# Kernel optimization log

Hardware: AMD Instinct MI355X
Metric: run time of the kernel (lower is better)

The kernel has to match this reference:

```python
import jax, jax.numpy as jnp
import numpy as np

LAMBDA_BOX = 5.0
LAMBDA_CLS = 1.0
NUM_CLASSES = 80


def setup_inputs() -> dict:
    key = jax.random.key(0)
    k1, k2, k3, k4, k5, k6 = jax.random.split(key, 6)
    B, P, T = 16, 16384, 64
    C = 5 + NUM_CLASSES
    raw = jax.random.normal(k1, (B, P, C), dtype=jnp.float32)
    # overwrite first 4 channels with valid xyxy boxes so IoU is meaningful
    p_xy = jax.random.uniform(k2, (B, P, 2), dtype=jnp.float32) * 448.0
    p_wh = jax.random.uniform(k3, (B, P, 2), dtype=jnp.float32) * 64.0 + 4.0
    raw = raw.at[..., :4].set(jnp.concatenate([p_xy, p_xy + p_wh], axis=-1))
    t_xy = jax.random.uniform(k4, (B, T, 2), dtype=jnp.float32) * 448.0
    t_wh = jax.random.uniform(k5, (B, T, 2), dtype=jnp.float32) * 64.0 + 4.0
    t_cls = jax.random.randint(k6, (B, T), 0, NUM_CLASSES).astype(jnp.float32)
    targets = jnp.concatenate([t_xy, t_xy + t_wh, t_cls[..., None]], axis=-1)
    return {"raw_preds": raw, "targets": targets, "epoch": 5}


def _iou_matrix(pb, tb):
    # pb: [B,P,4], tb: [B,T,4] -> IoU [B,P,T] (xyxy boxes)
    x1 = jnp.maximum(pb[:, :, None, 0], tb[:, None, :, 0])
    y1 = jnp.maximum(pb[:, :, None, 1], tb[:, None, :, 1])
    x2 = jnp.minimum(pb[:, :, None, 2], tb[:, None, :, 2])
    y2 = jnp.minimum(pb[:, :, None, 3], tb[:, None, :, 3])
    w = x2 - x1
    h = y2 - y1
    inter = w * h
    valid = (w > 0) & (h > 0)
    area_p = (pb[:, :, 2] - pb[:, :, 0]) * (pb[:, :, 3] - pb[:, :, 1])
    area_t = (tb[:, :, 2] - tb[:, :, 0]) * (tb[:, :, 3] - tb[:, :, 1])
    union = area_p[:, :, None] + area_t[:, None, :] - inter
    iou = jnp.where(valid & (union > 0), inter / jnp.where(union > 0, union, 1.0), 0.0)
    return iou


def _smooth_l1_sum(x, t):
    d = jnp.abs(x - t)
    return jnp.sum(jnp.where(d < 1.0, 0.5 * d * d, d - 0.5), axis=(-2, -1))


def _bce_logits_sum(x, t):
    # sum over last axis of BCEWithLogits
    return jnp.sum(jnp.logaddexp(0.0, x) - x * t, axis=-1)


def reference(raw_preds, targets, epoch):
    B, P, _ = raw_preds.shape
    T = targets.shape[1]
    # IoU is computed from detached numpy boxes in the original -> stop_gradient
    pb = jax.lax.stop_gradient(raw_preds[..., :4])
    tb = targets[..., :4]
    iou = _iou_matrix(pb, tb)                      # [B,P,T]
    # warmup branch (epoch < warmup_epochs): best pred per target
    matched_pred = jnp.argmax(iou, axis=1)         # [B,T]
    pred_pos_boxes = jnp.take_along_axis(raw_preds[..., :4], matched_pred[..., None], axis=1)  # [B,T,4]
    box_loss = _smooth_l1_sum(pred_pos_boxes, tb)  # [B]
    pred_pos_cls = jnp.take_along_axis(raw_preds[..., 5:], matched_pred[..., None], axis=1)    # [B,T,C]
    tcls = targets[..., 4].astype(jnp.int32)       # [B,T]
    logp = jax.nn.log_softmax(pred_pos_cls, axis=-1)
    cls_loss = -jnp.sum(jnp.take_along_axis(logp, tcls[..., None], axis=-1), axis=(-2, -1))    # [B]
    conf_target = jax.vmap(lambda idx: jnp.zeros((P,), jnp.float32).at[idx].set(1.0))(matched_pred)  # [B,P]
    conf_loss = _bce_logits_sum(raw_preds[..., 4], conf_target)  # [B]
    per_sample = LAMBDA_BOX * box_loss + LAMBDA_CLS * cls_loss + conf_loss
    return jnp.sum(per_sample) / B
```

## Files before the change

kernel.cpp:

```cpp
#include <hip/hip_runtime.h>
#include <math.h>

#define BB 16
#define PP 16384
#define TT 64
#define CC 85
#define WPW 64
#define PRED_PER_BLK 256
#define NSLOT 64

typedef float float4u __attribute__((ext_vector_type(4), aligned(4)));


__global__ __launch_bounds__(256) void pass1_kernel(const float* __restrict__ raw,
                                                    const float* __restrict__ tgt,
                                                    float2* __restrict__ cand,
                                                    float* __restrict__ conf_part) {
#pragma clang fp contract(off)
    int b     = blockIdx.x >> 6;
    int chunk = blockIdx.x & 63;
    int wave  = threadIdx.x >> 6;
    int lane  = threadIdx.x & 63;
    int p0    = chunk * PRED_PER_BLK + wave * WPW;

    __shared__ float4 sbox[4][WPW];
    __shared__ float  sarea[4][WPW];
    __shared__ float  sval[4][WPW];
    __shared__ int    sidx[4][WPW];
    __shared__ float  sconf[4];

    {
        const float* pr = raw + ((size_t)b * PP + p0 + lane) * CC;
        float4u bx = *(const float4u*)pr;
        float c = pr[4];
        sbox[wave][lane]  = make_float4(bx.x, bx.y, bx.z, bx.w);
        sarea[wave][lane] = (bx.z - bx.x) * (bx.w - bx.y);
        float ca = fmaxf(c, 0.0f) + log1pf(expf(-fabsf(c)));
        for (int m = 32; m > 0; m >>= 1) ca += __shfl_xor(ca, m);
        if (lane == 0) sconf[wave] = ca;
    }

    const float* trow = tgt + (size_t)(b * TT + lane) * 5;
    float tx1 = trow[0], ty1 = trow[1], tx2 = trow[2], ty2 = trow[3];
    float area_t = (tx2 - tx1) * (ty2 - ty1);

    float best = -1.0f;
    int bidx = 0;
#pragma unroll 4
    for (int j = 0; j < WPW; ++j) {
        float4 pb = sbox[wave][j];
        float ap  = sarea[wave][j];
        float x1 = fmaxf(pb.x, tx1), y1 = fmaxf(pb.y, ty1);
        float x2 = fminf(pb.z, tx2), y2 = fminf(pb.w, ty2);
        float w = x2 - x1, h = y2 - y1;
        float inter = w * h;
        bool valid = (w > 0.0f) && (h > 0.0f);
        float uni = (ap + area_t) - inter;
        float iou = (valid && (uni > 0.0f)) ? (inter / uni) : 0.0f;
        if (iou > best) { best = iou; bidx = p0 + j; }
    }
    sval[wave][lane] = best;
    sidx[wave][lane] = bidx;
    __syncthreads();

    if (threadIdx.x == 0)
        conf_part[blockIdx.x] = (sconf[0] + sconf[1]) + (sconf[2] + sconf[3]);

    if (wave == 0) {
        float v = sval[0][lane];
        int   i = sidx[0][lane];
        for (int w2 = 1; w2 < 4; ++w2) {
            float v2 = sval[w2][lane];
            int   i2 = sidx[w2][lane];
            if (v2 > v || (v2 == v && i2 < i)) { v = v2; i = i2; }
        }
        cand[(size_t)(b * TT + lane) * NSLOT + chunk] = make_float2(v, __int_as_float(i));
    }
}

__global__ __launch_bounds__(64) void pass2_kernel(const float* __restrict__ raw,
                                                   const float* __restrict__ tgt,
                                                   const float2* __restrict__ cand,
                                                   float* __restrict__ loss_bt,
                                                   int* __restrict__ matched) {
#pragma clang fp contract(off)
    int bt = blockIdx.x;
    int b = bt >> 6;
    int lane = threadIdx.x;

    float2 c2 = cand[(size_t)bt * NSLOT + lane];
    float v = c2.x;
    int idx = __float_as_int(c2.y);
    for (int m = 1; m < 64; m <<= 1) {
        float ov = __shfl_xor(v, m);
        int   oi = __shfl_xor(idx, m);
        if (ov > v || (ov == v && oi < idx)) { v = ov; idx = oi; }
    }
    const float* prow = raw + ((size_t)b * PP + idx) * CC;
    float l0 = prow[5 + lane];
    float l1 = (lane < 16) ? prow[69 + lane] : -INFINITY;
    float mx = fmaxf(l0, l1);
    for (int m = 1; m < 64; m <<= 1) mx = fmaxf(mx, __shfl_xor(mx, m));
    float e = expf(l0 - mx) + ((lane < 16) ? expf(l1 - mx) : 0.0f);
    for (int m = 1; m < 64; m <<= 1) e += __shfl_xor(e, m);

    if (lane == 0) {
        const float* trow = tgt + (size_t)bt * 5;
        int tcls = (int)trow[4];
        float cls = (mx + logf(e)) - prow[5 + tcls];
        float s = 0.0f;
        for (int k = 0; k < 4; ++k) {
            float d = fabsf(prow[k] - trow[k]);
            s += (d < 1.0f) ? 0.5f * d * d : (d - 0.5f);
        }
        loss_bt[bt] = 5.0f * s + cls;
        matched[bt] = idx;
    }
}

__global__ __launch_bounds__(256) void pass3_kernel(const float* __restrict__ raw,
                                                    const float* __restrict__ conf_part,
                                                    const float* __restrict__ loss_bt,
                                                    const int* __restrict__ matched,
                                                    float* __restrict__ out) {
    __shared__ int sm[BB * TT];
    __shared__ float red[256];
    int tid = threadIdx.x;
    for (int i = tid; i < BB * TT; i += 256) sm[i] = matched[i];
    __syncthreads();

    float acc = 0.0f;
    for (int i = tid; i < BB * TT; i += 256) {
        int m = sm[i];
        bool first = true;
        for (int t2 = i & ~63; t2 < i; ++t2)
            if (sm[t2] == m) { first = false; break; }
        int b = i >> 6;
        float sub = first ? raw[((size_t)b * PP + m) * CC + 4] : 0.0f;
        acc += loss_bt[i] - sub;
    }
    for (int i = tid; i < 1024; i += 256) acc += conf_part[i];

    red[tid] = acc;
    __syncthreads();
    for (int s = 128; s > 0; s >>= 1) {
        if (tid < s) red[tid] += red[tid + s];
        __syncthreads();
    }
    if (tid == 0) out[0] = red[0] / (float)BB;
}

extern "C" void kernel_launch(void* const* d_in, const int* in_sizes, int n_in,
                              void* d_out, int out_size, void* d_ws, size_t ws_size,
                              hipStream_t stream) {
    const float* raw = (const float*)d_in[0];
    const float* tgt = (const float*)d_in[1];
    float* out = (float*)d_out;
    float* wsf = (float*)d_ws;

    float2* cand    = (float2*)wsf;
    float*  conf_p  = wsf + 131072;
    float*  loss_bt = wsf + 132096;
    int*    match   = (int*)(wsf + 133120);

    pass1_kernel<<<BB * 64, 256, 0, stream>>>(raw, tgt, cand, conf_p);
    pass2_kernel<<<BB * TT, 64, 0, stream>>>(raw, tgt, cand, loss_bt, match);
    pass3_kernel<<<1, 256, 0, stream>>>(raw, conf_p, loss_bt, match, out);
}
```

Before: 53.25 us.

## Fuse pass2 and pass3 into single-block tail kernel and double pass1 chunk size

Pass1 now handles 512 predictions per block, halving the block count and the number of candidate slots per target. It also stores candidates chunk-major so reads are coalesced. The former per-target pass2 and final reduction pass3 are merged into one 1024-thread kernel. In that kernel each thread reduces its target's candidates, computes the log-softmax and box loss with vectorized loads, handles the duplicate-match correction, and reduces everything. This removes a kernel launch and the intermediate workspace round trip. The cost is that all tail work runs on one block, with 80-wide per-thread loops and uncoalesced gathers.

```diff
diff --git a/kernel.cpp b/kernel.cpp
--- a/kernel.cpp
+++ b/kernel.cpp
@@ -5,9 +5,9 @@
 #define PP 16384
 #define TT 64
 #define CC 85
-#define WPW 64
-#define PRED_PER_BLK 256
-#define NSLOT 64
+#define PRED_PER_BLK 512
+#define CHUNKS (PP / PRED_PER_BLK)
+#define NBLK1 (BB * CHUNKS)
 
 typedef float float4u __attribute__((ext_vector_type(4), aligned(4)));
 
@@ -17,28 +17,32 @@
                                                     float2* __restrict__ cand,
                                                     float* __restrict__ conf_part) {
 #pragma clang fp contract(off)
-    int b     = blockIdx.x >> 6;
-    int chunk = blockIdx.x & 63;
-    int wave  = threadIdx.x >> 6;
-    int lane  = threadIdx.x & 63;
-    int p0    = chunk * PRED_PER_BLK + wave * WPW;
+    int b     = blockIdx.x / CHUNKS;
+    int chunk = blockIdx.x % CHUNKS;
+    int p0    = chunk * PRED_PER_BLK;
+    int tid   = threadIdx.x;
+    int wave  = tid >> 6, lane = tid & 63;
 
-    __shared__ float4 sbox[4][WPW];
-    __shared__ float  sarea[4][WPW];
-    __shared__ float  sval[4][WPW];
-    __shared__ int    sidx[4][WPW];
+    __shared__ float4 sbox[PRED_PER_BLK];
+    __shared__ float  sarea[PRED_PER_BLK];
+    __shared__ float  sval[4][64];
+    __shared__ int    sidx[4][64];
     __shared__ float  sconf[4];
 
-    {
-        const float* pr = raw + ((size_t)b * PP + p0 + lane) * CC;
+    const float* base = raw + (size_t)b * PP * CC;
+
+    float ca = 0.0f;
+    for (int r = tid; r < PRED_PER_BLK; r += 256) {
+        const float* pr = base + (size_t)(p0 + r) * CC;
         float4u bx = *(const float4u*)pr;
         float c = pr[4];
-        sbox[wave][lane]  = make_float4(bx.x, bx.y, bx.z, bx.w);
-        sarea[wave][lane] = (bx.z - bx.x) * (bx.w - bx.y);
-        float ca = fmaxf(c, 0.0f) + log1pf(expf(-fabsf(c)));
-        for (int m = 32; m > 0; m >>= 1) ca += __shfl_xor(ca, m);
-        if (lane == 0) sconf[wave] = ca;
+        sbox[r]  = make_float4(bx.x, bx.y, bx.z, bx.w);
+        sarea[r] = (bx.z - bx.x) * (bx.w - bx.y);
+        ca += fmaxf(c, 0.0f) + log1pf(expf(-fabsf(c)));
     }
+    for (int m = 32; m > 0; m >>= 1) ca += __shfl_xor(ca, m);
+    if (lane == 0) sconf[wave] = ca;
+    __syncthreads();
 
     const float* trow = tgt + (size_t)(b * TT + lane) * 5;
     float tx1 = trow[0], ty1 = trow[1], tx2 = trow[2], ty2 = trow[3];
@@ -46,10 +50,11 @@
 
     float best = -1.0f;
     int bidx = 0;
+    int j0 = wave * (PRED_PER_BLK / 4);
 #pragma unroll 4
-    for (int j = 0; j < WPW; ++j) {
-        float4 pb = sbox[wave][j];
-        float ap  = sarea[wave][j];
+    for (int j = 0; j < PRED_PER_BLK / 4; ++j) {
+        float4 pb = sbox[j0 + j];
+        float ap  = sarea[j0 + j];
         float x1 = fmaxf(pb.x, tx1), y1 = fmaxf(pb.y, ty1);
         float x2 = fminf(pb.z, tx2), y2 = fminf(pb.w, ty2);
         float w = x2 - x1, h = y2 - y1;
@@ -57,14 +62,13 @@
         bool valid = (w > 0.0f) && (h > 0.0f);
         float uni = (ap + area_t) - inter;
         float iou = (valid && (uni > 0.0f)) ? (inter / uni) : 0.0f;
-        if (iou > best) { best = iou; bidx = p0 + j; }
+        if (iou > best) { best = iou; bidx = p0 + j0 + j; }
     }
     sval[wave][lane] = best;
     sidx[wave][lane] = bidx;
     __syncthreads();
 
-    if (threadIdx.x == 0)
-        conf_part[blockIdx.x] = (sconf[0] + sconf[1]) + (sconf[2] + sconf[3]);
+    if (tid == 0) conf_part[blockIdx.x] = (sconf[0] + sconf[1]) + (sconf[2] + sconf[3]);
 
     if (wave == 0) {
         float v = sval[0][lane];
@@ -74,80 +78,75 @@
             int   i2 = sidx[w2][lane];
             if (v2 > v || (v2 == v && i2 < i)) { v = v2; i = i2; }
         }
-        cand[(size_t)(b * TT + lane) * NSLOT + chunk] = make_float2(v, __int_as_float(i));
+        cand[((size_t)b * CHUNKS + chunk) * TT + lane] = make_float2(v, __int_as_float(i));
     }
 }
 
-__global__ __launch_bounds__(64) void pass2_kernel(const float* __restrict__ raw,
-                                                   const float* __restrict__ tgt,
-                                                   const float2* __restrict__ cand,
-                                                   float* __restrict__ loss_bt,
-                                                   int* __restrict__ matched) {
-#pragma clang fp contract(off)
-    int bt = blockIdx.x;
-    int b = bt >> 6;
-    int lane = threadIdx.x;
+__global__ __launch_bounds__(1024) void tail_kernel(const float* __restrict__ raw,
+                                                    const float* __restrict__ tgt,
+                                                    const float2* __restrict__ cand,
+                                                    const float* __restrict__ conf_part,
+                                                    float* __restrict__ out) {
+    int tid = threadIdx.x;
+    int b = tid >> 6;
 
-    float2 c2 = cand[(size_t)bt * NSLOT + lane];
-    float v = c2.x;
-    int idx = __float_as_int(c2.y);
-    for (int m = 1; m < 64; m <<= 1) {
-        float ov = __shfl_xor(v, m);
-        int   oi = __shfl_xor(idx, m);
-        if (ov > v || (ov == v && oi < idx)) { v = ov; idx = oi; }
+    __shared__ int   sm[BB * TT];
+    __shared__ float wsum[16];
+
+    float v = -2.0f;
+    int idx = 0x7fffffff;
+    for (int k = 0; k < CHUNKS; ++k) {
+        float2 c2 = cand[((size_t)b * CHUNKS + k) * TT + (tid & 63)];
+        int i2 = __float_as_int(c2.y);
+        if (c2.x > v || (c2.x == v && i2 < idx)) { v = c2.x; idx = i2; }
     }
+    sm[tid] = idx;
+
     const float* prow = raw + ((size_t)b * PP + idx) * CC;
-    float l0 = prow[5 + lane];
-    float l1 = (lane < 16) ? prow[69 + lane] : -INFINITY;
-    float mx = fmaxf(l0, l1);
-    for (int m = 1; m < 64; m <<= 1) mx = fmaxf(mx, __shfl_xor(mx, m));
-    float e = expf(l0 - mx) + ((lane < 16) ? expf(l1 - mx) : 0.0f);
-    for (int m = 1; m < 64; m <<= 1) e += __shfl_xor(e, m);
+    const float* trow = tgt + (size_t)tid * 5;
 
-    if (lane == 0) {
-        const float* trow = tgt + (size_t)bt * 5;
-        int tcls = (int)trow[4];
-        float cls = (mx + logf(e)) - prow[5 + tcls];
-        float s = 0.0f;
-        for (int k = 0; k < 4; ++k) {
-            float d = fabsf(prow[k] - trow[k]);
-            s += (d < 1.0f) ? 0.5f * d * d : (d - 0.5f);
-        }
-        loss_bt[bt] = 5.0f * s + cls;
-        matched[bt] = idx;
+    float4u lg[20];
+#pragma unroll
+    for (int k = 0; k < 20; ++k) lg[k] = *(const float4u*)(prow + 5 + 4 * k);
+    float mx = -INFINITY;
+#pragma unroll
+    for (int k = 0; k < 20; ++k)
+        mx = fmaxf(fmaxf(fmaxf(mx, lg[k].x), fmaxf(lg[k].y, lg[k].z)), lg[k].w);
+    float se = 0.0f;
+#pragma unroll
+    for (int k = 0; k < 20; ++k)
+        se += expf(lg[k].x - mx) + expf(lg[k].y - mx) + expf(lg[k].z - mx) + expf(lg[k].w - mx);
+    int tcls = (int)trow[4];
+    float cls = (mx + logf(se)) - prow[5 + tcls];
+
+    float4u pb = *(const float4u*)prow;
+    float box = 0.0f;
+    {
+        float d;
+        d = fabsf(pb.x - trow[0]); box += (d < 1.0f) ? 0.5f * d * d : (d - 0.5f);
+        d = fabsf(pb.y - trow[1]); box += (d < 1.0f) ? 0.5f * d * d : (d - 0.5f);
+        d = fabsf(pb.z - trow[2]); box += (d < 1.0f) ? 0.5f * d * d : (d - 0.5f);
+        d = fabsf(pb.w - trow[3]); box += (d < 1.0f) ? 0.5f * d * d : (d - 0.5f);
     }
-}
+    float acc = 5.0f * box + cls;
 
-__global__ __launch_bounds__(256) void pass3_kernel(const float* __restrict__ raw,
-                                                    const float* __restrict__ conf_part,
-                                                    const float* __restrict__ loss_bt,
-                                                    const int* __restrict__ matched,
-                                                    float* __restrict__ out) {
-    __shared__ int sm[BB * TT];
-    __shared__ float red[256];
-    int tid = threadIdx.x;
-    for (int i = tid; i < BB * TT; i += 256) sm[i] = matched[i];
     __syncthreads();
 
-    float acc = 0.0f;
-    for (int i = tid; i < BB * TT; i += 256) {
-        int m = sm[i];
-        bool first = true;
-        for (int t2 = i & ~63; t2 < i; ++t2)
-            if (sm[t2] == m) { first = false; break; }
-        int b = i >> 6;
-        float sub = first ? raw[((size_t)b * PP + m) * CC + 4] : 0.0f;
-        acc += loss_bt[i] - sub;
+    bool first = true;
+    for (int t2 = b * 64; t2 < tid; ++t2)
+        if (sm[t2] == idx) { first = false; break; }
+    if (first) acc -= prow[4];
+
+    if (tid < NBLK1) acc += conf_part[tid];
+
+    for (int m = 32; m > 0; m >>= 1) acc += __shfl_xor(acc, m);
+    if ((tid & 63) == 0) wsum[tid >> 6] = acc;
+    __syncthreads();
+    if (tid == 0) {
+        float s = 0.0f;
+        for (int w = 0; w < 16; ++w) s += wsum[w];
+        out[0] = s / (float)BB;
     }
-    for (int i = tid; i < 1024; i += 256) acc += conf_part[i];
-
-    red[tid] = acc;
-    __syncthreads();
-    for (int s = 128; s > 0; s >>= 1) {
-        if (tid < s) red[tid] += red[tid + s];
-        __syncthreads();
-    }
-    if (tid == 0) out[0] = red[0] / (float)BB;
 }
 
 extern "C" void kernel_launch(void* const* d_in, const int* in_sizes, int n_in,
@@ -158,12 +157,9 @@
     float* out = (float*)d_out;
     float* wsf = (float*)d_ws;
 
-    float2* cand    = (float2*)wsf;
-    float*  conf_p  = wsf + 131072;
-    float*  loss_bt = wsf + 132096;
-    int*    match   = (int*)(wsf + 133120);
+    float2* cand   = (float2*)wsf;
+    float*  conf_p = wsf + 65536;
 
-    pass1_kernel<<<BB * 64, 256, 0, stream>>>(raw, tgt, cand, conf_p);
-    pass2_kernel<<<BB * TT, 64, 0, stream>>>(raw, tgt, cand, loss_bt, match);
-    pass3_kernel<<<1, 256, 0, stream>>>(raw, conf_p, loss_bt, match, out);
+    pass1_kernel<<<NBLK1, 256, 0, stream>>>(raw, tgt, cand, conf_p);
+    tail_kernel<<<1, 1024, 0, stream>>>(raw, tgt, cand, conf_p, out);
 }
```

New measurement: 57.20 us. 1.07x slower.

## Fuse three passes into one persistent kernel with atomic grid barriers

Applied to the files above, without the earlier changes.

Merges the IoU/argmax pass, the per-target loss pass and the final reduction into one kernel launch of 512 blocks that synchronise through atomic-counter grid barriers, with a memset to reset the counters. Each block now covers 512 predictions instead of 256, and IoU comparison uses a division-free cross-multiplication that keeps intersection and union separately. This is meant to remove the launch gaps and tail effects between the three small kernels. In exchange it depends on all 512 blocks being co-resident to avoid deadlock, and it adds barrier spin cost, an extra memset node, and possible tie-breaking differences from the cross-multiplied comparison.

```diff
diff --git a/kernel.cpp b/kernel.cpp
--- a/kernel.cpp
+++ b/kernel.cpp
@@ -5,127 +5,140 @@
 #define PP 16384
 #define TT 64
 #define CC 85
-#define WPW 64
-#define PRED_PER_BLK 256
-#define NSLOT 64
+#define PRED_PER_BLK 512
+#define CHUNKS (PP / PRED_PER_BLK)
+#define NBLK (BB * CHUNKS)
 
 typedef float float4u __attribute__((ext_vector_type(4), aligned(4)));
 
 
-__global__ __launch_bounds__(256) void pass1_kernel(const float* __restrict__ raw,
-                                                    const float* __restrict__ tgt,
-                                                    float2* __restrict__ cand,
-                                                    float* __restrict__ conf_part) {
-#pragma clang fp contract(off)
-    int b     = blockIdx.x >> 6;
-    int chunk = blockIdx.x & 63;
-    int wave  = threadIdx.x >> 6;
-    int lane  = threadIdx.x & 63;
-    int p0    = chunk * PRED_PER_BLK + wave * WPW;
+__device__ __forceinline__ void gridbar(unsigned int* cnt) {
+    __syncthreads();
+    if (threadIdx.x == 0) {
+        __threadfence();
+        __hip_atomic_fetch_add(cnt, 1u, __ATOMIC_ACQ_REL, __HIP_MEMORY_SCOPE_AGENT);
+        unsigned int spins = 0;
+        while (__hip_atomic_load(cnt, __ATOMIC_ACQUIRE, __HIP_MEMORY_SCOPE_AGENT) < (unsigned)NBLK) {
+            __builtin_amdgcn_s_sleep(2);
+            if (++spins > 100000000u) break;
+        }
+        __threadfence();
+    }
+    __syncthreads();
+}
 
-    __shared__ float4 sbox[4][WPW];
-    __shared__ float  sarea[4][WPW];
-    __shared__ float  sval[4][WPW];
-    __shared__ int    sidx[4][WPW];
+__global__ __launch_bounds__(256, 2) void fused_kernel(const float* __restrict__ raw,
+                                                       const float* __restrict__ tgt,
+                                                       float* __restrict__ wsf,
+                                                       float* __restrict__ out) {
+    float2* cand    = (float2*)wsf;
+    float*  conf_p  = wsf + 65536;
+    float*  loss_bt = wsf + 66048;
+    int*    matched = (int*)(wsf + 67072);
+    unsigned int* bar = (unsigned int*)(wsf + 68096);
+
+    int tid  = threadIdx.x;
+    int wave = tid >> 6, lane = tid & 63;
+    int b     = blockIdx.x / CHUNKS;
+    int chunk = blockIdx.x % CHUNKS;
+    int p0    = chunk * PRED_PER_BLK;
+
+    __shared__ float4 sbox[PRED_PER_BLK];
+    __shared__ float  sbi[4][64], sbu[4][64];
+    __shared__ int    sbidx[4][64];
     __shared__ float  sconf[4];
+    __shared__ int    sm[BB * TT];
+    __shared__ float  wsum[4];
 
-    {
-        const float* pr = raw + ((size_t)b * PP + p0 + lane) * CC;
+    const float* base = raw + (size_t)b * PP * CC;
+    float ca = 0.0f;
+    for (int r = tid; r < PRED_PER_BLK; r += 256) {
+        const float* pr = base + (size_t)(p0 + r) * CC;
         float4u bx = *(const float4u*)pr;
         float c = pr[4];
-        sbox[wave][lane]  = make_float4(bx.x, bx.y, bx.z, bx.w);
-        sarea[wave][lane] = (bx.z - bx.x) * (bx.w - bx.y);
-        float ca = fmaxf(c, 0.0f) + log1pf(expf(-fabsf(c)));
-        for (int m = 32; m > 0; m >>= 1) ca += __shfl_xor(ca, m);
-        if (lane == 0) sconf[wave] = ca;
+        sbox[r] = make_float4(bx.x, bx.y, bx.z, bx.w);
+        ca += fmaxf(c, 0.0f) + log1pf(expf(-fabsf(c)));
     }
+    for (int m = 32; m > 0; m >>= 1) ca += __shfl_xor(ca, m);
+    if (lane == 0) sconf[wave] = ca;
+    __syncthreads();
 
     const float* trow = tgt + (size_t)(b * TT + lane) * 5;
     float tx1 = trow[0], ty1 = trow[1], tx2 = trow[2], ty2 = trow[3];
     float area_t = (tx2 - tx1) * (ty2 - ty1);
 
-    float best = -1.0f;
-    int bidx = 0;
+    float bi = -1.0f, bu = 1.0f;
+    int bidx = p0;
+    int j0 = wave * (PRED_PER_BLK / 4);
 #pragma unroll 4
-    for (int j = 0; j < WPW; ++j) {
-        float4 pb = sbox[wave][j];
-        float ap  = sarea[wave][j];
+    for (int j = 0; j < PRED_PER_BLK / 4; ++j) {
+        float4 pb = sbox[j0 + j];
+        float ap = (pb.z - pb.x) * (pb.w - pb.y);
         float x1 = fmaxf(pb.x, tx1), y1 = fmaxf(pb.y, ty1);
         float x2 = fminf(pb.z, tx2), y2 = fminf(pb.w, ty2);
         float w = x2 - x1, h = y2 - y1;
         float inter = w * h;
-        bool valid = (w > 0.0f) && (h > 0.0f);
         float uni = (ap + area_t) - inter;
-        float iou = (valid && (uni > 0.0f)) ? (inter / uni) : 0.0f;
-        if (iou > best) { best = iou; bidx = p0 + j; }
+        bool ok = (w > 0.0f) && (h > 0.0f) && (uni > 0.0f);
+        float ie = ok ? inter : 0.0f;
+        float ue = ok ? uni : 1.0f;
+        if (ie * bu > bi * ue) { bi = ie; bu = ue; bidx = p0 + j0 + j; }
     }
-    sval[wave][lane] = best;
-    sidx[wave][lane] = bidx;
+    sbi[wave][lane] = bi; sbu[wave][lane] = bu; sbidx[wave][lane] = bidx;
     __syncthreads();
 
-    if (threadIdx.x == 0)
-        conf_part[blockIdx.x] = (sconf[0] + sconf[1]) + (sconf[2] + sconf[3]);
+    if (tid == 0) conf_p[blockIdx.x] = (sconf[0] + sconf[1]) + (sconf[2] + sconf[3]);
 
     if (wave == 0) {
-        float v = sval[0][lane];
-        int   i = sidx[0][lane];
+        float i1 = sbi[0][lane], u1 = sbu[0][lane];
+        int ix = sbidx[0][lane];
         for (int w2 = 1; w2 < 4; ++w2) {
-            float v2 = sval[w2][lane];
-            int   i2 = sidx[w2][lane];
-            if (v2 > v || (v2 == v && i2 < i)) { v = v2; i = i2; }
+            float i2 = sbi[w2][lane], u2 = sbu[w2][lane];
+            if (i2 * u1 > i1 * u2) { i1 = i2; u1 = u2; ix = sbidx[w2][lane]; }
         }
-        cand[(size_t)(b * TT + lane) * NSLOT + chunk] = make_float2(v, __int_as_float(i));
+        float iou = fmaxf(i1, 0.0f) / u1;
+        cand[((size_t)b * CHUNKS + chunk) * TT + lane] = make_float2(iou, __int_as_float(ix));
     }
-}
 
-__global__ __launch_bounds__(64) void pass2_kernel(const float* __restrict__ raw,
-                                                   const float* __restrict__ tgt,
-                                                   const float2* __restrict__ cand,
-                                                   float* __restrict__ loss_bt,
-                                                   int* __restrict__ matched) {
-#pragma clang fp contract(off)
-    int bt = blockIdx.x;
-    int b = bt >> 6;
-    int lane = threadIdx.x;
+    gridbar(&bar[0]);
 
-    float2 c2 = cand[(size_t)bt * NSLOT + lane];
-    float v = c2.x;
-    int idx = __float_as_int(c2.y);
-    for (int m = 1; m < 64; m <<= 1) {
-        float ov = __shfl_xor(v, m);
-        int   oi = __shfl_xor(idx, m);
-        if (ov > v || (ov == v && oi < idx)) { v = ov; idx = oi; }
+    if (wave < 2) {
+        int bt = blockIdx.x * 2 + wave;
+        int b2 = bt >> 6, t2 = bt & 63;
+        float v = -2.0f; int idx = 0x7fffffff;
+        if (lane < CHUNKS) {
+            float2 c2 = cand[((size_t)b2 * CHUNKS + lane) * TT + t2];
+            v = c2.x; idx = __float_as_int(c2.y);
+        }
+        for (int m = 1; m < 64; m <<= 1) {
+            float ov = __shfl_xor(v, m); int oi = __shfl_xor(idx, m);
+            if (ov > v || (ov == v && oi < idx)) { v = ov; idx = oi; }
+        }
+        const float* prow = raw + ((size_t)b2 * PP + idx) * CC;
+        float l0 = prow[5 + lane];
+        float l1 = (lane < 16) ? prow[69 + lane] : -INFINITY;
+        float mx = fmaxf(l0, l1);
+        for (int m = 1; m < 64; m <<= 1) mx = fmaxf(mx, __shfl_xor(mx, m));
+        float e = expf(l0 - mx) + ((lane < 16) ? expf(l1 - mx) : 0.0f);
+        for (int m = 1; m < 64; m <<= 1) e += __shfl_xor(e, m);
+        if (lane == 0) {
+            const float* tr2 = tgt + (size_t)bt * 5;
+            int tcls = (int)tr2[4];
+            float cls = (mx + logf(e)) - prow[5 + tcls];
+            float bxl = 0.0f;
+            for (int k = 0; k < 4; ++k) {
+                float d = fabsf(prow[k] - tr2[k]);
+                bxl += (d < 1.0f) ? 0.5f * d * d : (d - 0.5f);
+            }
+            loss_bt[bt] = 5.0f * bxl + cls;
+            matched[bt] = idx;
+        }
     }
-    const float* prow = raw + ((size_t)b * PP + idx) * CC;
-    float l0 = prow[5 + lane];
-    float l1 = (lane < 16) ? prow[69 + lane] : -INFINITY;
-    float mx = fmaxf(l0, l1);
-    for (int m = 1; m < 64; m <<= 1) mx = fmaxf(mx, __shfl_xor(mx, m));
-    float e = expf(l0 - mx) + ((lane < 16) ? expf(l1 - mx) : 0.0f);
-    for (int m = 1; m < 64; m <<= 1) e += __shfl_xor(e, m);
 
-    if (lane == 0) {
-        const float* trow = tgt + (size_t)bt * 5;
-        int tcls = (int)trow[4];
-        float cls = (mx + logf(e)) - prow[5 + tcls];
-        float s = 0.0f;
-        for (int k = 0; k < 4; ++k) {
-            float d = fabsf(prow[k] - trow[k]);
-            s += (d < 1.0f) ? 0.5f * d * d : (d - 0.5f);
-        }
-        loss_bt[bt] = 5.0f * s + cls;
-        matched[bt] = idx;
-    }
-}
+    gridbar(&bar[1]);
 
-__global__ __launch_bounds__(256) void pass3_kernel(const float* __restrict__ raw,
-                                                    const float* __restrict__ conf_part,
-                                                    const float* __restrict__ loss_bt,
-                                                    const int* __restrict__ matched,
-                                                    float* __restrict__ out) {
-    __shared__ int sm[BB * TT];
-    __shared__ float red[256];
-    int tid = threadIdx.x;
+    if (blockIdx.x != NBLK - 1) return;
+
     for (int i = tid; i < BB * TT; i += 256) sm[i] = matched[i];
     __syncthreads();
 
@@ -133,21 +146,17 @@
     for (int i = tid; i < BB * TT; i += 256) {
         int m = sm[i];
         bool first = true;
-        for (int t2 = i & ~63; t2 < i; ++t2)
-            if (sm[t2] == m) { first = false; break; }
-        int b = i >> 6;
-        float sub = first ? raw[((size_t)b * PP + m) * CC + 4] : 0.0f;
+        for (int t3 = i & ~63; t3 < i; ++t3)
+            if (sm[t3] == m) { first = false; break; }
+        float sub = first ? raw[((size_t)(i >> 6) * PP + m) * CC + 4] : 0.0f;
         acc += loss_bt[i] - sub;
     }
-    for (int i = tid; i < 1024; i += 256) acc += conf_part[i];
+    for (int i = tid; i < NBLK; i += 256) acc += conf_p[i];
 
-    red[tid] = acc;
+    for (int m = 32; m > 0; m >>= 1) acc += __shfl_xor(acc, m);
+    if (lane == 0) wsum[wave] = acc;
     __syncthreads();
-    for (int s = 128; s > 0; s >>= 1) {
-        if (tid < s) red[tid] += red[tid + s];
-        __syncthreads();
-    }
-    if (tid == 0) out[0] = red[0] / (float)BB;
+    if (tid == 0) out[0] = ((wsum[0] + wsum[1]) + (wsum[2] + wsum[3])) / (float)BB;
 }
 
 extern "C" void kernel_launch(void* const* d_in, const int* in_sizes, int n_in,
@@ -158,12 +167,6 @@
     float* out = (float*)d_out;
     float* wsf = (float*)d_ws;
 
-    float2* cand    = (float2*)wsf;
-    float*  conf_p  = wsf + 131072;
-    float*  loss_bt = wsf + 132096;
-    int*    match   = (int*)(wsf + 133120);
-
-    pass1_kernel<<<BB * 64, 256, 0, stream>>>(raw, tgt, cand, conf_p);
-    pass2_kernel<<<BB * TT, 64, 0, stream>>>(raw, tgt, cand, loss_bt, match);
-    pass3_kernel<<<1, 256, 0, stream>>>(raw, conf_p, loss_bt, match, out);
+    hipMemsetAsync(wsf + 68096, 0, 8, stream);
+    fused_kernel<<<NBLK, 256, 0, stream>>>(raw, tgt, wsf, out);
 }
```

Measured after the change: 149.3 us. +180.4%, slower.
